# Kernel tuning notes

Hardware: AMD Instinct MI355X
Metric: run time of the kernel (lower is better)

The kernel has to match this reference:

```python
import jax, jax.numpy as jnp
import numpy as np

D_MODEL = 512
NUM_HEADS = 8
HEAD_DIM = 64  # D_MODEL // NUM_HEADS


def setup_inputs() -> dict:
    key = jax.random.key(0)
    kq, kk, kv, kw, kb = jax.random.split(key, 5)
    B, S = 2, 2048
    query = jax.random.normal(kq, (B, S, D_MODEL), dtype=jnp.float32)
    key_t = jax.random.normal(kk, (B, S, D_MODEL), dtype=jnp.float32)
    value = jax.random.normal(kv, (B, S, D_MODEL), dtype=jnp.float32)
    # shared projection (nn.Linear(d_models, d_models)) applied to q, k, v
    scale = 1.0 / np.sqrt(D_MODEL)
    W = jax.random.uniform(kw, (D_MODEL, D_MODEL), dtype=jnp.float32, minval=-scale, maxval=scale)
    b = jax.random.uniform(kb, (D_MODEL,), dtype=jnp.float32, minval=-scale, maxval=scale)
    return {"query": query, "key": key_t, "value": value, "W": W, "b": b}


def reference(query, key, value, W, b):
    B, S, _ = query.shape
    H, Dh = NUM_HEADS, HEAD_DIM

    def proj(x):  # nn.Linear + ReLU, shared across q/k/v
        return jax.nn.relu(jnp.einsum('bsd,ed->bse', x, W) + b)

    # [B, S, d] -> [B, H, S, Dh]
    split = lambda x: proj(x).reshape(B, S, H, Dh).transpose(0, 2, 1, 3)
    Q, K, V = split(query), split(key), split(value)

    scores = jnp.einsum('bhqd,bhkd->bhqk', Q, K) / jnp.sqrt(jnp.float32(Dh))
    causal_mask = jnp.triu(jnp.ones((S, S), dtype=bool), k=1)  # True above diagonal
    scores = jnp.where(causal_mask, -jnp.inf, scores)
    attn = jax.nn.softmax(scores, axis=-1)
    out = jnp.einsum('bhqk,bhkd->bhqd', attn, V)  # [B, H, S, Dh]

    # faithful to original: transpose(0,1) swaps batch and heads, then view
    final = jnp.swapaxes(out, 0, 1).reshape(B, -1, D_MODEL)  # [B, S, d_model]
    return final
```

## Files before the change

### kernel.cpp

```cpp
#include <hip/hip_runtime.h>
#include <hip/hip_bf16.h>
#include <cstdint>
#include <cstddef>

typedef __bf16 bf16_t;
typedef bf16_t bf16x8 __attribute__((ext_vector_type(8)));
typedef float f32x4 __attribute__((ext_vector_type(4)));
typedef float f32x16 __attribute__((ext_vector_type(16)));
typedef unsigned short u16;
typedef u16 u16x8 __attribute__((ext_vector_type(8)));

#define S_LEN 2048
#define NB 2
#define NH 8
#define DHD 64
#define DM 512

static __device__ __forceinline__ u16 bfbits(float f) {
  union { __bf16 h; u16 u; } c; c.h = (__bf16)f; return c.u;
}
static __device__ __forceinline__ float bits2f(u16 b) {
  union { u16 u; __bf16 h; } c; c.u = b; return (float)c.h;
}
static __device__ __forceinline__ uint32_t pkbf(float a, float b) {
  union { __bf16 h[2]; uint32_t u; } c;
  c.h[0] = (__bf16)a; c.h[1] = (__bf16)b;
  return c.u;
}
static __device__ __forceinline__ void gload16(const void* g, void* l) {
  __builtin_amdgcn_global_load_lds(
      (const __attribute__((address_space(1))) uint32_t*)g,
      (__attribute__((address_space(3))) uint32_t*)l, 16, 0, 0);
}

static __device__ __forceinline__ int slot_of(int bh, int t32, int chunk) {
  int qb = t32 >> 2;
  int nc = (2 * (qb + 1) + 9) / 10;
  int off;
  if (qb < 10) off = (qb - 5) * 8;
  else if (qb < 15) off = 40 + (qb - 10) * 12;
  else off = 100;
  return bh * 116 + off + (t32 & 3) * nc + chunk;
}

__launch_bounds__(256, 2)
__global__ void proj_kernel(const float* __restrict__ Xq, const float* __restrict__ Xk,
                            const float* __restrict__ Xv, const float* __restrict__ W,
                            const float* __restrict__ bias,
                            u16* __restrict__ Qw, u16* __restrict__ Kw,
                            u16* __restrict__ Vt64) {
  __shared__ __align__(16) float BUF[2][8192];
  const int bid = blockIdx.x;
  const int xcd = bid & 7;
  const int u = bid >> 3;
  const int n0 = (u & 3) * 128;
  const int mIdx = u >> 2;
  const int mg = (xcd * 12 + mIdx) * 128;
  const int z = mg >> 12;
  const int m_in = mg & 4095;
  const int b = m_in >> 11;
  const int s0m = m_in & (S_LEN - 1);
  const int h0 = n0 >> 6;
  const float* __restrict__ X = (z == 0) ? Xq : ((z == 1) ? Xk : Xv);
  X += (size_t)m_in * DM;

  const int t = threadIdx.x;
  const int lane = t & 63;
  const int wid = t >> 6;
  const int wr = wid >> 1, wc = wid & 1;
  const int fr = lane & 15, fg = lane >> 4;

  f32x4 acc[4][4] = {};

  const int lrow = lane >> 3;
  const int lblk = lane & 7;

  auto stage = [&](int bf, int k0) {
    #pragma unroll
    for (int i = 0; i < 4; ++i) {
      int c = wid * 4 + i;
      int r = c * 8 + lrow;
      gload16(X + (size_t)r * DM + k0 + ((lblk ^ (r & 7)) << 2), &BUF[bf][c * 256]);
    }
    #pragma unroll
    for (int i = 0; i < 4; ++i) {
      int c = wid * 4 + i;
      int r = c * 8 + lrow;
      gload16(W + (size_t)(n0 + r) * DM + k0 + ((lblk ^ (r & 7)) << 2),
              &BUF[bf][4096 + c * 256]);
    }
  };

  stage(0, 0);
  int cb = 0;
  for (int i = 0; i < 16; ++i) {
    __syncthreads();
    if (i < 15) stage(cb ^ 1, (i + 1) * 32);
    const float* Ac = BUF[cb];
    bf16x8 af[4], bfr[4];
    #pragma unroll
    for (int m2 = 0; m2 < 4; ++m2) {
      int r = wr*64 + m2*16 + fr;
      f32x4 lo = *(const f32x4*)&Ac[r*32 + (((2*fg)     ^ (r & 7)) << 2)];
      f32x4 hi = *(const f32x4*)&Ac[r*32 + (((2*fg + 1) ^ (r & 7)) << 2)];
      union { u16x8 s; bf16x8 v; } f;
      f.s[0]=bfbits(lo[0]); f.s[1]=bfbits(lo[1]); f.s[2]=bfbits(lo[2]); f.s[3]=bfbits(lo[3]);
      f.s[4]=bfbits(hi[0]); f.s[5]=bfbits(hi[1]); f.s[6]=bfbits(hi[2]); f.s[7]=bfbits(hi[3]);
      af[m2] = f.v;
    }
    #pragma unroll
    for (int ni = 0; ni < 4; ++ni) {
      int r = wc*64 + ni*16 + fr;
      f32x4 lo = *(const f32x4*)&Ac[4096 + r*32 + (((2*fg)     ^ (r & 7)) << 2)];
      f32x4 hi = *(const f32x4*)&Ac[4096 + r*32 + (((2*fg + 1) ^ (r & 7)) << 2)];
      union { u16x8 s; bf16x8 v; } f;
      f.s[0]=bfbits(lo[0]); f.s[1]=bfbits(lo[1]); f.s[2]=bfbits(lo[2]); f.s[3]=bfbits(lo[3]);
      f.s[4]=bfbits(hi[0]); f.s[5]=bfbits(hi[1]); f.s[6]=bfbits(hi[2]); f.s[7]=bfbits(hi[3]);
      bfr[ni] = f.v;
    }
    __builtin_amdgcn_s_setprio(1);
    #pragma unroll
    for (int m2 = 0; m2 < 4; ++m2)
      #pragma unroll
      for (int ni = 0; ni < 4; ++ni)
        acc[m2][ni] = __builtin_amdgcn_mfma_f32_16x16x32_bf16(af[m2], bfr[ni], acc[m2][ni], 0, 0, 0);
    __builtin_amdgcn_s_setprio(0);
    cb ^= 1;
  }
  __syncthreads();

  const float QSCALE = 0.125f * 1.44269504089f;
  u16* epi = (u16*)&BUF[0][0];

  if (z == 2) {
    #pragma unroll
    for (int m2 = 0; m2 < 4; ++m2) {
      #pragma unroll
      for (int ni = 0; ni < 4; ++ni) {
        int e = wc*64 + ni*16 + fr;
        int m = wr*64 + m2*16 + fg*4;
        float bv = bias[n0 + e];
        float v0 = fmaxf(acc[m2][ni][0] + bv, 0.f);
        float v1 = fmaxf(acc[m2][ni][1] + bv, 0.f);
        float v2 = fmaxf(acc[m2][ni][2] + bv, 0.f);
        float v3 = fmaxf(acc[m2][ni][3] + bv, 0.f);
        uint2 w; w.x = pkbf(v0, v1); w.y = pkbf(v2, v3);
        *(uint2*)&epi[e*136 + m] = w;
      }
    }
    __syncthreads();
    const int e2 = t >> 1, mc = (t & 1) * 64;
    const int h = h0 + (e2 >> 6), d = e2 & 63;
    const int sb = (s0m >> 6) + (mc >> 6);
    u16* dst = Vt64 + (((size_t)(b * NH + h) * 32 + sb) * 64 + d) * 64;
    #pragma unroll
    for (int i = 0; i < 8; ++i)
      *(uint4*)(dst + i*8) = *(const uint4*)&epi[e2*136 + mc + i*8];
  } else {
    #pragma unroll
    for (int m2 = 0; m2 < 4; ++m2) {
      #pragma unroll
      for (int ni = 0; ni < 4; ++ni) {
        int e = wc*64 + ni*16 + fr;
        float bv = bias[n0 + e];
        #pragma unroll
        for (int r = 0; r < 4; ++r) {
          float v = acc[m2][ni][r] + bv;
          if (z == 0) v *= QSCALE;
          v = fmaxf(v, 0.f);
          epi[(wr*64 + m2*16 + fg*4 + r)*136 + e] = bfbits(v);
        }
      }
    }
    __syncthreads();
    const int mrow = t >> 1, hf = t & 1;
    u16* dst = ((z == 0) ? Qw : Kw) +
               (((size_t)(b * NH + h0 + hf)) * S_LEN + s0m + mrow) * DHD;
    #pragma unroll
    for (int i = 0; i < 8; ++i)
      *(uint4*)(dst + i*8) = *(const uint4*)&epi[mrow*136 + hf*64 + i*8];
  }
}

static __device__ const uint8_t QBT[34] = {4,5,6,7,8,9,9,10,10,11,11,12,12,13,13,14,14,14,15,15,15,
                                           3,8,13, 2,7,12, 1,6,11, 0,5,10,15};
static __device__ const uint8_t CKT[34] = {0,0,0,0,0,0,1,0,1,0,1,0,1,0,1,0,1,2,0,1,2,
                                           0,1,2, 0,1,2, 0,1,2, 0,1,2,3};

__launch_bounds__(256, 2)
__global__ void attn_kernel(const u16* __restrict__ Qw, const u16* __restrict__ Kw,
                            const u16* __restrict__ Vt64, u16* __restrict__ Opart,
                            float* __restrict__ lbuf, float* __restrict__ out) {
  __shared__ u16 KLDS[4][4096];
  __shared__ u16 VLDS[4][4096];
  const int t = threadIdx.x;
  const int lane = t & 63;
  const int wid = t >> 6;
  const int lam = lane & 31;
  const int hi = lane >> 5;
  const int h8 = hi << 3, h4 = hi << 2;
  const int bid = blockIdx.x;
  const int bh = bid & 15;
  const int u = bid >> 4;
  const int qb = QBT[u], chunk = CKT[u];
  const int steps_total = (qb + 1) * 2;
  const int sc0 = chunk * 10;
  const int sc1e = sc0 + 10;
  const int sc1 = (sc1e < steps_total) ? sc1e : steps_total;
  const int t32 = qb * 4 + wid;
  const int q0 = qb * 128 + wid * 32;

  const u16* __restrict__ Qh = Qw + (size_t)bh * S_LEN * DHD;
  const u16* __restrict__ Kh = Kw + (size_t)bh * S_LEN * DHD;
  const u16* __restrict__ V64 = Vt64 + (size_t)bh * 32 * 64 * 64;

  bf16x8 qf[4];
  #pragma unroll
  for (int c = 0; c < 4; ++c)
    qf[c] = *(const bf16x8*)(Qh + (size_t)(q0 + lam) * DHD + c*16 + h8);

  const int lrow = lane >> 3;
  const int lblk = lane & 7;
  auto stage = [&](int bf, int s) {
    #pragma unroll
    for (int i = 0; i < 2; ++i) {
      int c = wid * 2 + i;
      int r = c * 8 + lrow;
      int sw = (lblk ^ (r & 7)) << 3;
      gload16(Kh + (size_t)(s * 64 + r) * 64 + sw, &KLDS[bf][c * 512]);
      gload16(V64 + ((size_t)s * 64 + r) * 64 + sw, &VLDS[bf][c * 512]);
    }
  };

  f32x16 o0 = {}, o1 = {};
  float lsum = 0.f;

  auto softpack = [&](const f32x16& sc, bool msk, bf16x8& pb0v, bf16x8& pb1v) {
    float p[16];
    #pragma unroll
    for (int r = 0; r < 16; ++r) {
      float ev = __builtin_amdgcn_exp2f(sc[r]);
      int kc = (r & 3) + ((r >> 2) << 3) + h4;
      if (msk && kc > lam) ev = 0.f;
      p[r] = ev;
      lsum += ev;
    }
    uint32_t X0 = pkbf(p[0], p[1]),  X1 = pkbf(p[2], p[3]);
    uint32_t X2 = pkbf(p[4], p[5]),  X3 = pkbf(p[6], p[7]);
    uint32_t X4 = pkbf(p[8], p[9]),  X5 = pkbf(p[10], p[11]);
    uint32_t X6 = pkbf(p[12], p[13]), X7 = pkbf(p[14], p[15]);
    asm("v_permlane32_swap_b32 %0, %1" : "+v"(X0), "+v"(X2));
    asm("v_permlane32_swap_b32 %0, %1" : "+v"(X1), "+v"(X3));
    asm("v_permlane32_swap_b32 %0, %1" : "+v"(X4), "+v"(X6));
    asm("v_permlane32_swap_b32 %0, %1" : "+v"(X5), "+v"(X7));
    union U8 { uint32_t u[4]; bf16x8 v; };
    U8 a, bU;
    a.u[0] = X0; a.u[1] = X1; a.u[2] = X2; a.u[3] = X3;
    bU.u[0] = X4; bU.u[1] = X5; bU.u[2] = X6; bU.u[3] = X7;
    pb0v = a.v; pb1v = bU.v;
  };

  auto do_step = [&](int s, int buf) {
    const int d2 = t32 - 2 * s;
    if (d2 < 0) return;
    if (d2 >= 1) {
      bf16x8 kA[4], kB[4];
      #pragma unroll
      for (int c = 0; c < 4; ++c) {
        int rA = lam,      eA = ((2*c + hi) ^ (rA & 7)) * 8;
        int rB = 32 + lam, eB = ((2*c + hi) ^ (rB & 7)) * 8;
        kA[c] = *(const bf16x8*)&KLDS[buf][rA*64 + eA];
        kB[c] = *(const bf16x8*)&KLDS[buf][rB*64 + eB];
      }
      f32x16 sA = {}, sB = {};
      __builtin_amdgcn_s_setprio(1);
      #pragma unroll
      for (int c = 0; c < 4; ++c) {
        sA = __builtin_amdgcn_mfma_f32_32x32x16_bf16(kA[c], qf[c], sA, 0, 0, 0);
        sB = __builtin_amdgcn_mfma_f32_32x32x16_bf16(kB[c], qf[c], sB, 0, 0, 0);
      }
      __builtin_amdgcn_s_setprio(0);
      bf16x8 a0, a1, b0v, b1v;
      softpack(sA, false, a0, a1);
      softpack(sB, d2 == 1, b0v, b1v);
      bf16x8 vA0[2], vA1[2], vB0[2], vB1[2];
      #pragma unroll
      for (int c2 = 0; c2 < 2; ++c2) {
        int r0 = lam, r1 = 32 + lam;
        vA0[c2] = *(const bf16x8*)&VLDS[buf][r0*64 + (((2*c2 + hi) ^ (r0 & 7)) * 8)];
        vA1[c2] = *(const bf16x8*)&VLDS[buf][r1*64 + (((2*c2 + hi) ^ (r1 & 7)) * 8)];
        vB0[c2] = *(const bf16x8*)&VLDS[buf][r0*64 + (((4 + 2*c2 + hi) ^ (r0 & 7)) * 8)];
        vB1[c2] = *(const bf16x8*)&VLDS[buf][r1*64 + (((4 + 2*c2 + hi) ^ (r1 & 7)) * 8)];
      }
      __builtin_amdgcn_s_setprio(1);
      o0 = __builtin_amdgcn_mfma_f32_32x32x16_bf16(vA0[0], a0, o0, 0, 0, 0);
      o1 = __builtin_amdgcn_mfma_f32_32x32x16_bf16(vA1[0], a0, o1, 0, 0, 0);
      o0 = __builtin_amdgcn_mfma_f32_32x32x16_bf16(vA0[1], a1, o0, 0, 0, 0);
      o1 = __builtin_amdgcn_mfma_f32_32x32x16_bf16(vA1[1], a1, o1, 0, 0, 0);
      o0 = __builtin_amdgcn_mfma_f32_32x32x16_bf16(vB0[0], b0v, o0, 0, 0, 0);
      o1 = __builtin_amdgcn_mfma_f32_32x32x16_bf16(vB1[0], b0v, o1, 0, 0, 0);
      o0 = __builtin_amdgcn_mfma_f32_32x32x16_bf16(vB0[1], b1v, o0, 0, 0, 0);
      o1 = __builtin_amdgcn_mfma_f32_32x32x16_bf16(vB1[1], b1v, o1, 0, 0, 0);
      __builtin_amdgcn_s_setprio(0);
    } else {
      bf16x8 kA[4];
      #pragma unroll
      for (int c = 0; c < 4; ++c) {
        int r = lam, e = ((2*c + hi) ^ (r & 7)) * 8;
        kA[c] = *(const bf16x8*)&KLDS[buf][r*64 + e];
      }
      f32x16 sA = {};
      __builtin_amdgcn_s_setprio(1);
      #pragma unroll
      for (int c = 0; c < 4; ++c)
        sA = __builtin_amdgcn_mfma_f32_32x32x16_bf16(kA[c], qf[c], sA, 0, 0, 0);
      __builtin_amdgcn_s_setprio(0);
      bf16x8 a0, a1;
      softpack(sA, true, a0, a1);
      bf16x8 v0[2], v1[2];
      #pragma unroll
      for (int c2 = 0; c2 < 2; ++c2) {
        int r0 = lam,      e0 = ((2*c2 + hi) ^ (r0 & 7)) * 8;
        int r1 = 32 + lam, e1 = ((2*c2 + hi) ^ (r1 & 7)) * 8;
        v0[c2] = *(const bf16x8*)&VLDS[buf][r0*64 + e0];
        v1[c2] = *(const bf16x8*)&VLDS[buf][r1*64 + e1];
      }
      __builtin_amdgcn_s_setprio(1);
      o0 = __builtin_amdgcn_mfma_f32_32x32x16_bf16(v0[0], a0, o0, 0, 0, 0);
      o1 = __builtin_amdgcn_mfma_f32_32x32x16_bf16(v1[0], a0, o1, 0, 0, 0);
      o0 = __builtin_amdgcn_mfma_f32_32x32x16_bf16(v0[1], a1, o0, 0, 0, 0);
      o1 = __builtin_amdgcn_mfma_f32_32x32x16_bf16(v1[1], a1, o1, 0, 0, 0);
      __builtin_amdgcn_s_setprio(0);
    }
  };

  stage(0, sc0);
  stage(1, sc0 + 1);
  int ib = 0;
  for (int s = sc0; s < sc1; s += 2) {
    __syncthreads();
    if (s + 2 < sc1) {
      stage((ib + 2) & 3, s + 2);
      stage((ib + 3) & 3, s + 3);
    }
    do_step(s, ib);
    do_step(s + 1, (ib + 1) & 3);
    ib = (ib + 2) & 3;
  }

  float l = lsum + __shfl_xor(lsum, 32);

  if (qb <= 4) {
    const int b = bh >> 3, hh = bh & 7;
    const float inv = 1.0f / l;
    float* orow = out + (((size_t)(hh * NB + b)) * S_LEN + (q0 + lam)) * DHD;
    #pragma unroll
    for (int r = 0; r < 16; ++r) {
      int d = (r & 3) + ((r >> 2) << 3) + h4;
      orow[d] = o0[r] * inv;
      orow[d + 32] = o1[r] * inv;
    }
  } else {
    const int slot = slot_of(bh, t32, chunk);
    uint32_t w[16] __attribute__((aligned(16)));
    #pragma unroll
    for (int m = 0; m < 8; ++m) {
      w[m]     = pkbf(o0[2*m], o0[2*m+1]);
      w[8 + m] = pkbf(o1[2*m], o1[2*m+1]);
    }
    u16* op = Opart + (size_t)slot * 2048 + (size_t)lane * 32;
    #pragma unroll
    for (int i = 0; i < 4; ++i)
      *(uint4*)(op + i*8) = *(const uint4*)&w[i*4];
    if (lane < 32) lbuf[slot * 32 + lane] = l;
  }
}

__launch_bounds__(256)
__global__ void reduce_kernel(const u16* __restrict__ Opart,
                              const float* __restrict__ lbuf,
                              float* __restrict__ out) {
  const int t = threadIdx.x;
  const int unit = blockIdx.x * 4 + (t >> 6);
  const int bh = unit & 15;
  const int ti = 20 + (unit >> 4);
  const int qb = ti >> 2;
  const int nc = (2 * (qb + 1) + 9) / 10;
  const int lane = t & 63;
  const int lam = lane & 31;
  const int h4 = (lane >> 5) << 2;
  const int slot0 = slot_of(bh, ti, 0);

  float O[32];
  #pragma unroll
  for (int i = 0; i < 32; ++i) O[i] = 0.f;
  float L = 0.f;

  for (int c = 0; c < nc; ++c) {
    const u16* op = Opart + (size_t)(slot0 + c) * 2048 + (size_t)lane * 32;
    L += lbuf[(slot0 + c) * 32 + lam];
    #pragma unroll
    for (int i = 0; i < 4; ++i) {
      uint4 v = *(const uint4*)(op + i*8);
      uint32_t a[4] = {v.x, v.y, v.z, v.w};
      #pragma unroll
      for (int jj = 0; jj < 4; ++jj) {
        O[i*8 + 2*jj]     += bits2f((u16)(a[jj] & 0xFFFFu));
        O[i*8 + 2*jj + 1] += bits2f((u16)(a[jj] >> 16));
      }
    }
  }

  const int b = bh >> 3, hh = bh & 7;
  const float inv = 1.0f / L;
  float* orow = out + (((size_t)(hh * NB + b)) * S_LEN + (ti*32 + lam)) * DHD;
  #pragma unroll
  for (int r = 0; r < 16; ++r) {
    int d = (r & 3) + ((r >> 2) << 3) + h4;
    orow[d] = O[r] * inv;
    orow[d + 32] = O[16 + r] * inv;
  }
}

extern "C" void kernel_launch(void* const* d_in, const int* in_sizes, int n_in,
                              void* d_out, int out_size, void* d_ws, size_t ws_size,
                              hipStream_t stream) {
  const float* q = (const float*)d_in[0];
  const float* k = (const float*)d_in[1];
  const float* v = (const float*)d_in[2];
  const float* W = (const float*)d_in[3];
  const float* b = (const float*)d_in[4];

  const size_t elems = (size_t)NB * NH * S_LEN * DHD;
  u16* Qw = (u16*)d_ws;
  u16* Kw = Qw + elems;
  u16* Vt64 = Kw + elems;
  u16* Opart = Vt64 + elems;
  float* lbuf = (float*)(Opart + (size_t)1856 * 2048);

  proj_kernel<<<dim3(384), dim3(256), 0, stream>>>(q, k, v, W, b, Qw, Kw, Vt64);

  attn_kernel<<<dim3(544), dim3(256), 0, stream>>>(Qw, Kw, Vt64, Opart, lbuf, (float*)d_out);

  reduce_kernel<<<dim3(176), dim3(256), 0, stream>>>(Opart, lbuf, (float*)d_out);
}
```

Measured before the change: 47.76 us.

## Interleave next step's QK MFMAs with current step's PV MFMAs in attention loop

Adds a fused two-step path for fully or nearly unmasked tile pairs. The QK^T MFMAs of the second step are interleaved with the PV MFMAs of the first, and its K fragments are loaded early, so softmax and pack latency overlaps with matrix work. The aim is to hide the dependency stall between score computation and accumulation. The cost is higher register pressure from more live fragments and accumulators, which could lower occupancy or cause spills.

```diff
diff --git a/kernel.cpp b/kernel.cpp
--- a/kernel.cpp
+++ b/kernel.cpp
@@ -260,18 +260,30 @@
     pb0v = a.v; pb1v = bU.v;
   };
 
+  auto loadK = [&](int buf, int half, bf16x8* k4) {
+    #pragma unroll
+    for (int c = 0; c < 4; ++c) {
+      int r = half * 32 + lam, e = ((2*c + hi) ^ (r & 7)) * 8;
+      k4[c] = *(const bf16x8*)&KLDS[buf][r*64 + e];
+    }
+  };
+  auto loadV = [&](int buf, int off, bf16x8* v0, bf16x8* v1) {
+    #pragma unroll
+    for (int c2 = 0; c2 < 2; ++c2) {
+      int r0 = lam,      e0 = ((off + 2*c2 + hi) ^ (r0 & 7)) * 8;
+      int r1 = 32 + lam, e1 = ((off + 2*c2 + hi) ^ (r1 & 7)) * 8;
+      v0[c2] = *(const bf16x8*)&VLDS[buf][r0*64 + e0];
+      v1[c2] = *(const bf16x8*)&VLDS[buf][r1*64 + e1];
+    }
+  };
+
   auto do_step = [&](int s, int buf) {
     const int d2 = t32 - 2 * s;
     if (d2 < 0) return;
     if (d2 >= 1) {
       bf16x8 kA[4], kB[4];
-      #pragma unroll
-      for (int c = 0; c < 4; ++c) {
-        int rA = lam,      eA = ((2*c + hi) ^ (rA & 7)) * 8;
-        int rB = 32 + lam, eB = ((2*c + hi) ^ (rB & 7)) * 8;
-        kA[c] = *(const bf16x8*)&KLDS[buf][rA*64 + eA];
-        kB[c] = *(const bf16x8*)&KLDS[buf][rB*64 + eB];
-      }
+      loadK(buf, 0, kA);
+      loadK(buf, 1, kB);
       f32x16 sA = {}, sB = {};
       __builtin_amdgcn_s_setprio(1);
       #pragma unroll
@@ -284,14 +296,8 @@
       softpack(sA, false, a0, a1);
       softpack(sB, d2 == 1, b0v, b1v);
       bf16x8 vA0[2], vA1[2], vB0[2], vB1[2];
-      #pragma unroll
-      for (int c2 = 0; c2 < 2; ++c2) {
-        int r0 = lam, r1 = 32 + lam;
-        vA0[c2] = *(const bf16x8*)&VLDS[buf][r0*64 + (((2*c2 + hi) ^ (r0 & 7)) * 8)];
-        vA1[c2] = *(const bf16x8*)&VLDS[buf][r1*64 + (((2*c2 + hi) ^ (r1 & 7)) * 8)];
-        vB0[c2] = *(const bf16x8*)&VLDS[buf][r0*64 + (((4 + 2*c2 + hi) ^ (r0 & 7)) * 8)];
-        vB1[c2] = *(const bf16x8*)&VLDS[buf][r1*64 + (((4 + 2*c2 + hi) ^ (r1 & 7)) * 8)];
-      }
+      loadV(buf, 0, vA0, vA1);
+      loadV(buf, 4, vB0, vB1);
       __builtin_amdgcn_s_setprio(1);
       o0 = __builtin_amdgcn_mfma_f32_32x32x16_bf16(vA0[0], a0, o0, 0, 0, 0);
       o1 = __builtin_amdgcn_mfma_f32_32x32x16_bf16(vA1[0], a0, o1, 0, 0, 0);
@@ -304,11 +310,7 @@
       __builtin_amdgcn_s_setprio(0);
     } else {
       bf16x8 kA[4];
-      #pragma unroll
-      for (int c = 0; c < 4; ++c) {
-        int r = lam, e = ((2*c + hi) ^ (r & 7)) * 8;
-        kA[c] = *(const bf16x8*)&KLDS[buf][r*64 + e];
-      }
+      loadK(buf, 0, kA);
       f32x16 sA = {};
       __builtin_amdgcn_s_setprio(1);
       #pragma unroll
@@ -318,13 +320,7 @@
       bf16x8 a0, a1;
       softpack(sA, true, a0, a1);
       bf16x8 v0[2], v1[2];
-      #pragma unroll
-      for (int c2 = 0; c2 < 2; ++c2) {
-        int r0 = lam,      e0 = ((2*c2 + hi) ^ (r0 & 7)) * 8;
-        int r1 = 32 + lam, e1 = ((2*c2 + hi) ^ (r1 & 7)) * 8;
-        v0[c2] = *(const bf16x8*)&VLDS[buf][r0*64 + e0];
-        v1[c2] = *(const bf16x8*)&VLDS[buf][r1*64 + e1];
-      }
+      loadV(buf, 0, v0, v1);
       __builtin_amdgcn_s_setprio(1);
       o0 = __builtin_amdgcn_mfma_f32_32x32x16_bf16(v0[0], a0, o0, 0, 0, 0);
       o1 = __builtin_amdgcn_mfma_f32_32x32x16_bf16(v1[0], a0, o1, 0, 0, 0);
@@ -332,6 +328,64 @@
       o1 = __builtin_amdgcn_mfma_f32_32x32x16_bf16(v1[1], a1, o1, 0, 0, 0);
       __builtin_amdgcn_s_setprio(0);
     }
+  };
+
+  auto fused_pair = [&](int b0i, int b1i, bool maskB1) {
+    bf16x8 kA0[4], kB0[4];
+    loadK(b0i, 0, kA0);
+    loadK(b0i, 1, kB0);
+    f32x16 sA0 = {}, sB0 = {};
+    __builtin_amdgcn_s_setprio(1);
+    #pragma unroll
+    for (int c = 0; c < 4; ++c) {
+      sA0 = __builtin_amdgcn_mfma_f32_32x32x16_bf16(kA0[c], qf[c], sA0, 0, 0, 0);
+      sB0 = __builtin_amdgcn_mfma_f32_32x32x16_bf16(kB0[c], qf[c], sB0, 0, 0, 0);
+    }
+    __builtin_amdgcn_s_setprio(0);
+    bf16x8 a00, a01, b00, b01;
+    softpack(sA0, false, a00, a01);
+    softpack(sB0, false, b00, b01);
+    bf16x8 kA1[4], kB1[4];
+    loadK(b1i, 0, kA1);
+    loadK(b1i, 1, kB1);
+    bf16x8 vA0[2], vA1[2], vB0[2], vB1[2];
+    loadV(b0i, 0, vA0, vA1);
+    loadV(b0i, 4, vB0, vB1);
+    f32x16 sA1 = {}, sB1 = {};
+    __builtin_amdgcn_s_setprio(1);
+    o0  = __builtin_amdgcn_mfma_f32_32x32x16_bf16(vA0[0], a00, o0, 0, 0, 0);
+    sA1 = __builtin_amdgcn_mfma_f32_32x32x16_bf16(kA1[0], qf[0], sA1, 0, 0, 0);
+    o1  = __builtin_amdgcn_mfma_f32_32x32x16_bf16(vA1[0], a00, o1, 0, 0, 0);
+    sB1 = __builtin_amdgcn_mfma_f32_32x32x16_bf16(kB1[0], qf[0], sB1, 0, 0, 0);
+    o0  = __builtin_amdgcn_mfma_f32_32x32x16_bf16(vA0[1], a01, o0, 0, 0, 0);
+    sA1 = __builtin_amdgcn_mfma_f32_32x32x16_bf16(kA1[1], qf[1], sA1, 0, 0, 0);
+    o1  = __builtin_amdgcn_mfma_f32_32x32x16_bf16(vA1[1], a01, o1, 0, 0, 0);
+    sB1 = __builtin_amdgcn_mfma_f32_32x32x16_bf16(kB1[1], qf[1], sB1, 0, 0, 0);
+    o0  = __builtin_amdgcn_mfma_f32_32x32x16_bf16(vB0[0], b00, o0, 0, 0, 0);
+    sA1 = __builtin_amdgcn_mfma_f32_32x32x16_bf16(kA1[2], qf[2], sA1, 0, 0, 0);
+    o1  = __builtin_amdgcn_mfma_f32_32x32x16_bf16(vB1[0], b00, o1, 0, 0, 0);
+    sB1 = __builtin_amdgcn_mfma_f32_32x32x16_bf16(kB1[2], qf[2], sB1, 0, 0, 0);
+    o0  = __builtin_amdgcn_mfma_f32_32x32x16_bf16(vB0[1], b01, o0, 0, 0, 0);
+    sA1 = __builtin_amdgcn_mfma_f32_32x32x16_bf16(kA1[3], qf[3], sA1, 0, 0, 0);
+    o1  = __builtin_amdgcn_mfma_f32_32x32x16_bf16(vB1[1], b01, o1, 0, 0, 0);
+    sB1 = __builtin_amdgcn_mfma_f32_32x32x16_bf16(kB1[3], qf[3], sB1, 0, 0, 0);
+    __builtin_amdgcn_s_setprio(0);
+    bf16x8 a10, a11, b10, b11;
+    softpack(sA1, false, a10, a11);
+    softpack(sB1, maskB1, b10, b11);
+    bf16x8 wA0[2], wA1[2], wB0[2], wB1[2];
+    loadV(b1i, 0, wA0, wA1);
+    loadV(b1i, 4, wB0, wB1);
+    __builtin_amdgcn_s_setprio(1);
+    o0 = __builtin_amdgcn_mfma_f32_32x32x16_bf16(wA0[0], a10, o0, 0, 0, 0);
+    o1 = __builtin_amdgcn_mfma_f32_32x32x16_bf16(wA1[0], a10, o1, 0, 0, 0);
+    o0 = __builtin_amdgcn_mfma_f32_32x32x16_bf16(wA0[1], a11, o0, 0, 0, 0);
+    o1 = __builtin_amdgcn_mfma_f32_32x32x16_bf16(wA1[1], a11, o1, 0, 0, 0);
+    o0 = __builtin_amdgcn_mfma_f32_32x32x16_bf16(wB0[0], b10, o0, 0, 0, 0);
+    o1 = __builtin_amdgcn_mfma_f32_32x32x16_bf16(wB1[0], b10, o1, 0, 0, 0);
+    o0 = __builtin_amdgcn_mfma_f32_32x32x16_bf16(wB0[1], b11, o0, 0, 0, 0);
+    o1 = __builtin_amdgcn_mfma_f32_32x32x16_bf16(wB1[1], b11, o1, 0, 0, 0);
+    __builtin_amdgcn_s_setprio(0);
   };
 
   stage(0, sc0);
@@ -343,8 +397,13 @@
       stage((ib + 2) & 3, s + 2);
       stage((ib + 3) & 3, s + 3);
     }
-    do_step(s, ib);
-    do_step(s + 1, (ib + 1) & 3);
+    const int d2s = t32 - 2 * s;
+    if (d2s >= 3) {
+      fused_pair(ib, (ib + 1) & 3, d2s == 3);
+    } else {
+      do_step(s, ib);
+      do_step(s + 1, (ib + 1) & 3);
+    }
     ib = (ib + 2) & 3;
   }
 
```

Result: no change. 47.45 us, median of 2 (-0.6%).
